# Kernel optimization log

Measured on AMD Instinct MI355X. Metric: run time of the kernel, lower is better.

## Reference

```python
import jax, jax.numpy as jnp
import numpy as np

B, NQ, NC, D, C = 8, 1024, 4096, 256, 24  # batch, n_query, n_context, emb_dim, num_classes


def setup_inputs() -> dict:
    key = jax.random.key(0)
    ks = jax.random.split(key, 11)
    sc = 0.05  # param init scale
    return {
        "q_head": jax.random.normal(ks[0], (B, NQ, D), jnp.float32),
        "q_tail": jax.random.normal(ks[1], (B, NQ, D), jnp.float32),
        "c_head": jax.random.normal(ks[2], (B, NC, D), jnp.float32),
        "c_tail": jax.random.normal(ks[3], (B, NC, D), jnp.float32),
        "context_labels": jax.random.randint(ks[4], (B, NC), 0, C + 1),
        "mask": jnp.ones((B, NC), jnp.float32),
        "W_rel": jax.random.normal(ks[5], (2 * D, D), jnp.float32) * sc,
        "b_rel": jnp.zeros((D,), jnp.float32),
        "W_gen": jax.random.normal(ks[6], (D, C + 1), jnp.float32) * sc,
        "b_gen": jnp.zeros((C + 1,), jnp.float32),
        "W_cp": jax.random.normal(ks[7], (2 * D, 1), jnp.float32) * sc,
        "b_cp": jnp.zeros((1,), jnp.float32),
    }


def reference(q_head, q_tail, c_head, c_tail, context_labels, mask,
              W_rel, b_rel, W_gen, b_gen, W_cp, b_cp):
    def rel_emb(h, t):
        return jnp.concatenate([h, t], axis=-1) @ W_rel + b_rel

    q_emb = rel_emb(q_head, q_tail)            # [B, NQ, D]
    c_emb = rel_emb(c_head, c_tail)            # [B, NC, D]

    # generate distribution
    gen_dist = jax.nn.log_softmax(q_emb @ W_gen + b_gen, axis=-1)  # [B, NQ, C+1]

    # attention distribution (copy)
    scores = jnp.einsum('bqd,bjd->bqj', q_emb, c_emb) * mask[:, None, :]  # [B, NQ, NC]
    lsm = jax.nn.log_softmax(scores, axis=-1)
    probs = jnp.exp(lsm)
    context_vec = jnp.einsum('bqj,bjd->bqd', probs, c_emb)  # [B, NQ, D]

    # grouped logsumexp over context labels == log(sum of softmax probs per class);
    # empty classes give log(0) = -inf, matching the original -inf mask + logsumexp.
    onehot = jax.nn.one_hot(context_labels, C + 1, dtype=probs.dtype)  # [B, NC, C+1]
    copy_dist = jnp.log(jnp.einsum('bqj,bjc->bqc', probs, onehot))     # [B, NQ, C+1]

    # should-copy gate
    logits = (jnp.concatenate([q_emb, context_vec], axis=-1) @ W_cp + b_cp)[..., 0]  # [B, NQ]
    copy_prob = jax.nn.log_sigmoid(logits)[..., None]
    gen_prob = jax.nn.log_sigmoid(-logits)[..., None]

    return jnp.logaddexp(copy_prob + copy_dist, gen_prob + gen_dist)  # [B, NQ, C+1]
```

## Files before the change

kernel.cpp:

```cpp
#include <hip/hip_runtime.h>


typedef __attribute__((ext_vector_type(8))) _Float16 half8;
typedef __attribute__((ext_vector_type(4))) float floatx4;

#define WB 8
#define WNQ 1024
#define WNC 4096
#define NROWS 8192

static __device__ __forceinline__ float logsig(float x) {
    return (x >= 0.f) ? -log1pf(__expf(-x)) : x - log1pf(__expf(x));
}

union V16h { int4 v; half8 h8; _Float16 h[8]; unsigned short s[8]; uint2 u2[2]; };
union F8   { float4 v[2]; float f[8]; };
union H4   { _Float16 h[4]; uint2 u; unsigned short s[4]; };

static __device__ __forceinline__ void async_lds16(const _Float16* g, _Float16* l) {
    __builtin_amdgcn_global_load_lds(
        (const __attribute__((address_space(1))) unsigned int*)g,
        (__attribute__((address_space(3))) unsigned int*)l,
        16, 0, 0);
}

__global__ void wprep_kernel(const float* __restrict__ Wrel,
                             const float* __restrict__ Wgen,
                             const float* __restrict__ Wcp,
                             _Float16* __restrict__ WT,
                             _Float16* __restrict__ GenB)
{
    const int bx = blockIdx.x;
    if (bx < 256) {
        const int n = bx;
        for (int k = threadIdx.x; k < 512; k += 256)
            WT[(long)n * 512 + k] = (_Float16)Wrel[(long)k * 256 + n];
    } else {
        const int n = bx - 256;
        const int k = threadIdx.x;
        float v = 0.f;
        if (n < 25)       v = Wgen[(long)k * 25 + n];
        else if (n == 25) v = Wcp[k];
        GenB[(long)n * 256 + k] = (_Float16)v;
    }
}

__global__ __launch_bounds__(256, 3) void emb_kernel(
    const float* __restrict__ q_head, const float* __restrict__ q_tail,
    const float* __restrict__ c_head, const float* __restrict__ c_tail,
    const _Float16* __restrict__ WT,
    const float* __restrict__ brel,
    _Float16* __restrict__ Qf, _Float16* __restrict__ Cf,
    _Float16* __restrict__ CfT)
{
    __shared__ _Float16 sA[2][2048];

    const int tid  = threadIdx.x;
    const int lane = tid & 63;
    const int wv   = tid >> 6;
    const int l15  = lane & 15;
    const int quad = lane >> 4;
    const int n0   = wv * 64;

    const float* head; const float* tail; _Float16* Ef;
    long m0; bool isQ;
    if (blockIdx.x < 128) {
        isQ = true;  head = q_head; tail = q_tail; Ef = Qf;
        m0 = (long)blockIdx.x * 64;
    } else {
        isQ = false; head = c_head; tail = c_tail; Ef = Cf;
        m0 = (long)(blockIdx.x - 128) * 64;
    }

    const long arow = m0 + (tid >> 2);
    const int  akc  = (tid & 3) * 8;

    floatx4 acc[4][4];
#pragma unroll
    for (int a = 0; a < 4; ++a)
#pragma unroll
        for (int bq = 0; bq < 4; ++bq) acc[a][bq] = (floatx4)(0.0f);

    F8 aCur;
    aCur.v[0] = *(const float4*)(head + arow * 256 + akc);
    aCur.v[1] = *(const float4*)(head + arow * 256 + akc + 4);
    V16h wCur[4];
#pragma unroll
    for (int nt = 0; nt < 4; ++nt)
        wCur[nt].v = *(const int4*)(WT + (long)(n0 + nt * 16 + l15) * 512 + quad * 8);

    for (int ks = 0; ks < 16; ++ks) {
        {
            V16h hp;
#pragma unroll
            for (int i = 0; i < 8; ++i) hp.h[i] = (_Float16)aCur.f[i];
            *(int4*)&sA[ks & 1][tid * 8] = hp.v;
        }
        F8 aNxt; V16h wNxt[4];
        if (ks < 15) {
            const int kg = (ks + 1) * 32;
            const float* srcb = (kg < 256) ? (head + kg) : (tail + (kg - 256));
            aNxt.v[0] = *(const float4*)(srcb + arow * 256 + akc);
            aNxt.v[1] = *(const float4*)(srcb + arow * 256 + akc + 4);
#pragma unroll
            for (int nt = 0; nt < 4; ++nt)
                wNxt[nt].v = *(const int4*)(WT + (long)(n0 + nt * 16 + l15) * 512 + kg + quad * 8);
        } else {
            aNxt = aCur;
#pragma unroll
            for (int nt = 0; nt < 4; ++nt) wNxt[nt] = wCur[nt];
        }
        __syncthreads();

        V16h af[4];
#pragma unroll
        for (int mb = 0; mb < 4; ++mb)
            af[mb].v = *(const int4*)&sA[ks & 1][(mb * 16 + l15) * 32 + quad * 8];
#pragma unroll
        for (int mb = 0; mb < 4; ++mb)
#pragma unroll
            for (int nt = 0; nt < 4; ++nt)
                acc[mb][nt] = __builtin_amdgcn_mfma_f32_16x16x32_f16(af[mb].h8, wCur[nt].h8, acc[mb][nt], 0, 0, 0);

        aCur = aNxt;
#pragma unroll
        for (int nt = 0; nt < 4; ++nt) wCur[nt] = wNxt[nt];
    }

    float bias[4];
#pragma unroll
    for (int nt = 0; nt < 4; ++nt) bias[nt] = brel[n0 + nt * 16 + l15];

    const int bidx = (int)(m0 >> 12);
    const int jc0  = (int)(m0 & 4095);
#pragma unroll
    for (int mb = 0; mb < 4; ++mb)
#pragma unroll
        for (int nt = 0; nt < 4; ++nt)
#pragma unroll
            for (int r = 0; r < 4; ++r) {
                const long row = m0 + mb * 16 + quad * 4 + r;
                const _Float16 h = (_Float16)(acc[mb][nt][r] + bias[nt]);
                Ef[row * 256 + n0 + nt * 16 + l15] = h;
                if (!isQ) {
                    const int jc = jc0 + mb * 16 + quad * 4 + r;
                    CfT[(long)bidx * 1048576 + (long)(n0 + nt * 16 + l15) * 4096 + jc] = h;
                }
            }
}

__global__ __launch_bounds__(256, 4) void gen_kernel(
    const _Float16* __restrict__ Qf,
    const _Float16* __restrict__ GenB,
    const float* __restrict__ bgen,
    float* __restrict__ genlog)
{
    const int tid  = threadIdx.x;
    const int lane = tid & 63;
    const int wv   = tid >> 6;
    const int l15  = lane & 15;
    const int quad = lane >> 4;
    const long m0  = (long)blockIdx.x * 64 + wv * 16;

    floatx4 acc[2];
    acc[0] = (floatx4)(0.0f); acc[1] = (floatx4)(0.0f);
#pragma unroll
    for (int ks = 0; ks < 8; ++ks) {
        V16h a, b0, b1;
        a.v  = *(const int4*)(Qf + (m0 + l15) * 256 + ks * 32 + quad * 8);
        b0.v = *(const int4*)(GenB + (long)(l15)      * 256 + ks * 32 + quad * 8);
        b1.v = *(const int4*)(GenB + (long)(16 + l15) * 256 + ks * 32 + quad * 8);
        acc[0] = __builtin_amdgcn_mfma_f32_16x16x32_f16(a.h8, b0.h8, acc[0], 0, 0, 0);
        acc[1] = __builtin_amdgcn_mfma_f32_16x16x32_f16(a.h8, b1.h8, acc[1], 0, 0, 0);
    }
#pragma unroll
    for (int nt = 0; nt < 2; ++nt) {
        const int col = nt * 16 + l15;
        const float bias = (col < 25) ? bgen[col] : 0.f;
#pragma unroll
        for (int r = 0; r < 4; ++r)
            genlog[(m0 + quad * 4 + r) * 32 + col] = acc[nt][r] + bias;
    }
}

__global__ __launch_bounds__(256, 2) void attn_kernel(
    const _Float16* __restrict__ qf,
    const _Float16* __restrict__ cf,
    const _Float16* __restrict__ cfT,
    const int*      __restrict__ labels,
    const float*    __restrict__ maskp,
    unsigned short* __restrict__ Oh,
    float* __restrict__ Mst,
    float* __restrict__ Lst,
    int jtiles, int nsh)
{
    __shared__ _Float16 sA[2][8192];
    __shared__ _Float16 sB[2][8192];
    __shared__ _Float16 Pw[4][16 * 40];

    const int tid  = threadIdx.x;
    const int lane = tid & 63;
    const int wv   = tid >> 6;
    const int l15  = lane & 15;
    const int quad = lane >> 4;

    const int f   = blockIdx.x;
    const int xcd = f & 7;
    const int seq = f >> 3;
    const int qt  = seq & 15;
    const int u   = seq >> 4;
    const int pr  = u * 8 + xcd;
    const int b   = pr >> nsh;
    const int sp  = pr & ((1 << nsh) - 1);
    const int q0  = qt * 64;

    V16h qfr[8];
    {
        const long qrow = (long)b * WNQ + q0 + wv * 16 + l15;
#pragma unroll
        for (int ks = 0; ks < 8; ++ks)
            qfr[ks].v = *(const int4*)(qf + qrow * 256 + ks * 32 + quad * 8);
    }

    floatx4 O[18];
#pragma unroll
    for (int i = 0; i < 18; ++i) O[i] = (floatx4)(0.0f);
    float m_run = -INFINITY, l_run = 0.f;

    const int jb0 = sp * (jtiles * 32);

    auto stage = [&](int bf, int jb) {
        const long cbase = ((long)b * WNC + jb) * 256;
#pragma unroll
        for (int t = 0; t < 4; ++t) {
            const int idx = wv * 4 + t;
            const int ks = idx >> 1, jh = idx & 1;
            async_lds16(cf + cbase + (jh * 16 + l15) * 256 + ks * 32 + quad * 8,
                        &sA[bf][idx * 512]);
        }
        const long tbase = (long)b * 1048576 + jb;
#pragma unroll
        for (int t = 0; t < 4; ++t) {
            const int W = wv * 4 + t;
            async_lds16(cfT + tbase + (long)(W * 16 + (lane >> 2)) * 4096 + (lane & 3) * 8,
                        &sB[bf][W * 512]);
        }
    };

    stage(0, jb0);

    for (int it = 0; it < jtiles; ++it) {
        const int cur = it & 1;
        const int jb  = jb0 + it * 32;
        __syncthreads();
        if (it + 1 < jtiles) stage(cur ^ 1, jb + 32);

        const float4 mv0 = *(const float4*)(maskp + (long)b * WNC + jb + quad * 4);
        const float4 mv1 = *(const float4*)(maskp + (long)b * WNC + jb + 16 + quad * 4);
        const int4 lb0 = *(const int4*)(labels + (long)b * WNC + jb + quad * 8);
        const int4 lb1 = *(const int4*)(labels + (long)b * WNC + jb + quad * 8 + 4);

        floatx4 accS0 = (floatx4)(0.0f), accS1 = (floatx4)(0.0f);
#pragma unroll
        for (int ks = 0; ks < 8; ++ks) {
            V16h a0, a1;
            a0.v = *(const int4*)&sA[cur][(ks * 2 + 0) * 512 + (quad * 16 + l15) * 8];
            a1.v = *(const int4*)&sA[cur][(ks * 2 + 1) * 512 + (quad * 16 + l15) * 8];
            accS0 = __builtin_amdgcn_mfma_f32_16x16x32_f16(a0.h8, qfr[ks].h8, accS0, 0, 0, 0);
            accS1 = __builtin_amdgcn_mfma_f32_16x16x32_f16(a1.h8, qfr[ks].h8, accS1, 0, 0, 0);
        }
        const float* mv0p = (const float*)&mv0;
        const float* mv1p = (const float*)&mv1;
#pragma unroll
        for (int r = 0; r < 4; ++r) {
            accS0[r] *= mv0p[r];
            accS1[r] *= mv1p[r];
        }

        float v = fmaxf(fmaxf(fmaxf(accS0[0], accS0[1]), fmaxf(accS0[2], accS0[3])),
                        fmaxf(fmaxf(accS1[0], accS1[1]), fmaxf(accS1[2], accS1[3])));
        v = fmaxf(v, __shfl_xor(v, 16, 64));
        v = fmaxf(v, __shfl_xor(v, 32, 64));
        const float m_new = fmaxf(m_run, v);
        const float alpha = __expf(m_run - m_new);
        float p[8]; float ts = 0.f;
#pragma unroll
        for (int r = 0; r < 4; ++r) {
            p[r]     = __expf(accS0[r] - m_new); ts += p[r];
            p[4 + r] = __expf(accS1[r] - m_new); ts += p[4 + r];
        }
        ts += __shfl_xor(ts, 16, 64);
        ts += __shfl_xor(ts, 32, 64);
        l_run = l_run * alpha + ts;
        m_run = m_new;

        float ar[4];
#pragma unroll
        for (int r = 0; r < 4; ++r) ar[r] = __shfl(alpha, quad * 4 + r, 64);
#pragma unroll
        for (int fo = 0; fo < 18; ++fo)
#pragma unroll
            for (int r = 0; r < 4; ++r) O[fo][r] *= ar[r];

#pragma unroll
        for (int jf = 0; jf < 2; ++jf) {
            H4 w;
#pragma unroll
            for (int r = 0; r < 4; ++r) w.h[r] = (_Float16)p[jf * 4 + r];
            *(uint2*)&Pw[wv][l15 * 40 + jf * 16 + quad * 4] = w.u;
        }
        asm volatile("" ::: "memory");
        V16h pf;
        pf.v = *(const int4*)&Pw[wv][l15 * 40 + quad * 8];

        const int* lbp0 = (const int*)&lb0;
        const int* lbp1 = (const int*)&lb1;
        V16h oh0, oh1;
#pragma unroll
        for (int i = 0; i < 8; ++i) {
            const int lv = (i < 4) ? lbp0[i] : lbp1[i - 4];
            oh0.h[i] = (lv == l15)        ? (_Float16)1.0f : (_Float16)0.0f;
            oh1.h[i] = (lv == (l15 + 16)) ? (_Float16)1.0f : (_Float16)0.0f;
        }

#pragma unroll
        for (int dt = 0; dt < 16; ++dt) {
            V16h bfr;
            bfr.v = *(const int4*)&sB[cur][((dt * 16 + l15) * 4 + quad) * 8];
            O[dt] = __builtin_amdgcn_mfma_f32_16x16x32_f16(pf.h8, bfr.h8, O[dt], 0, 0, 0);
        }
        O[16] = __builtin_amdgcn_mfma_f32_16x16x32_f16(pf.h8, oh0.h8, O[16], 0, 0, 0);
        O[17] = __builtin_amdgcn_mfma_f32_16x16x32_f16(pf.h8, oh1.h8, O[17], 0, 0, 0);
    }

    {
        const long orow0 = (long)(sp * WB + b) * WNQ + q0 + wv * 16;
#pragma unroll
        for (int dt = 0; dt < 18; ++dt)
#pragma unroll
            for (int r = 0; r < 4; ++r) {
                H4 h; h.h[0] = (_Float16)O[dt][r];
                Oh[(orow0 + quad * 4 + r) * 288 + dt * 16 + l15] = h.s[0];
            }
        if (lane < 16) {
            const long sidx = (long)(sp * WB + b) * WNQ + q0 + wv * 16 + lane;
            Mst[sidx] = m_run;
            Lst[sidx] = l_run;
        }
    }
}

__global__ __launch_bounds__(256) void final_kernel(
    const float* __restrict__ genlog,
    const unsigned short* __restrict__ Oh,
    const float* __restrict__ Mst,
    const float* __restrict__ Lst,
    const float* __restrict__ Wcp,
    const float* __restrict__ bcp,
    float* __restrict__ outp,
    int ns)
{
    __shared__ float gA[4][32];
    __shared__ float cdA[4][32];

    const int tid  = threadIdx.x;
    const int lane = tid & 63;
    const int wv   = tid >> 6;
    const int row  = blockIdx.x * 4 + wv;

    float ms[8];
#pragma unroll
    for (int s = 0; s < 8; ++s) ms[s] = (s < ns) ? Mst[(long)s * NROWS + row] : -INFINITY;
    float mstar = -INFINITY;
#pragma unroll
    for (int s = 0; s < 8; ++s) mstar = fmaxf(mstar, ms[s]);
    float wgt[8]; float L = 0.f;
#pragma unroll
    for (int s = 0; s < 8; ++s) {
        wgt[s] = (ms[s] == -INFINITY) ? 0.f : __expf(ms[s] - mstar);
        if (s < ns) L += Lst[(long)s * NROWS + row] * wgt[s];
    }

    const int d0 = lane * 4;
    float ctx[4] = {0.f, 0.f, 0.f, 0.f};
#pragma unroll
    for (int s = 0; s < 8; ++s) {
        if (s < ns) {
            H4 t; t.u = *(const uint2*)&Oh[((long)s * NROWS + row) * 288 + d0];
#pragma unroll
            for (int i = 0; i < 4; ++i) ctx[i] += wgt[s] * (float)t.h[i];
        }
    }

    float cls[4] = {0.f, 0.f, 0.f, 0.f};
    if (lane < 8) {
#pragma unroll
        for (int s = 0; s < 8; ++s) {
            if (s < ns) {
                H4 t; t.u = *(const uint2*)&Oh[((long)s * NROWS + row) * 288 + 256 + lane * 4];
#pragma unroll
                for (int i = 0; i < 4; ++i) cls[i] += wgt[s] * (float)t.h[i];
            }
        }
    }

    float g = (lane < 25) ? genlog[(long)row * 32 + lane] : -INFINITY;
    float mg = g;
#pragma unroll
    for (int off = 32; off >= 1; off >>= 1) mg = fmaxf(mg, __shfl_xor(mg, off, 64));
    float se = (lane < 25) ? __expf(g - mg) : 0.f;
#pragma unroll
    for (int off = 32; off >= 1; off >>= 1) se += __shfl_xor(se, off, 64);
    const float glsm = g - mg - logf(se);

    const float qgate = genlog[(long)row * 32 + 25];
    const float invL = 1.f / L;
    float part = 0.f;
#pragma unroll
    for (int i = 0; i < 4; ++i)
        part += ctx[i] * invL * Wcp[256 + d0 + i];
#pragma unroll
    for (int off = 32; off >= 1; off >>= 1) part += __shfl_xor(part, off, 64);
    const float logit = qgate + part + bcp[0];

    const float lscp  = logsig(logit);
    const float lsgen = logsig(-logit);
    const float logL  = logf(L);

    if (lane < 8) {
#pragma unroll
        for (int i = 0; i < 4; ++i)
            cdA[wv][lane * 4 + i] = (cls[i] > 0.f) ? (logf(cls[i]) - logL) : -INFINITY;
    }
    if (lane < 25) gA[wv][lane] = glsm;
    __syncthreads();

    if (lane < 25) {
        const float a  = lscp + cdA[wv][lane];
        const float bb = lsgen + gA[wv][lane];
        const float mx = fmaxf(a, bb);
        const float o  = (mx == -INFINITY) ? -INFINITY
                         : mx + log1pf(__expf(fminf(a, bb) - mx));
        outp[(long)row * 25 + lane] = o;
    }
}

extern "C" void kernel_launch(void* const* d_in, const int* in_sizes, int n_in,
                              void* d_out, int out_size, void* d_ws, size_t ws_size,
                              hipStream_t stream) {
    const float* q_head = (const float*)d_in[0];
    const float* q_tail = (const float*)d_in[1];
    const float* c_head = (const float*)d_in[2];
    const float* c_tail = (const float*)d_in[3];
    const int*   labels = (const int*)d_in[4];
    const float* maskp  = (const float*)d_in[5];
    const float* Wrel   = (const float*)d_in[6];
    const float* brel   = (const float*)d_in[7];
    const float* Wgen   = (const float*)d_in[8];
    const float* bgen   = (const float*)d_in[9];
    const float* Wcp    = (const float*)d_in[10];
    const float* bcp    = (const float*)d_in[11];

    auto need = [](long ns) -> long { return 39075840l + ns * 4784128l; };
    int ns = 8, nsh = 3;
    if ((long)ws_size < need(8)) { ns = 4; nsh = 2; }
    if ((long)ws_size < need(4)) { ns = 2; nsh = 1; }
    if ((long)ws_size < need(2)) { ns = 1; nsh = 0; }
    const int jtiles = 128 / ns;

    char* ws = (char*)d_ws;
    _Float16* Qf     = (_Float16*)(ws);
    _Float16* Cf     = (_Float16*)(ws + 4194304l);
    _Float16* CfT    = (_Float16*)(ws + 20971520l);
    _Float16* WT     = (_Float16*)(ws + 37748736l);
    _Float16* GenB   = (_Float16*)(ws + 38010880l);
    float*    genlog = (float*)   (ws + 38027264l);
    unsigned short* Oh = (unsigned short*)(ws + 39075840l);
    float*    Mst    = (float*)   (ws + 39075840l + (long)ns * 4718592l);
    float*    Lst    = Mst + (long)ns * NROWS;

    hipLaunchKernelGGL(wprep_kernel, dim3(288), dim3(256), 0, stream,
                       Wrel, Wgen, Wcp, WT, GenB);
    hipLaunchKernelGGL(emb_kernel, dim3(640), dim3(256), 0, stream,
                       q_head, q_tail, c_head, c_tail, WT, brel, Qf, Cf, CfT);
    hipLaunchKernelGGL(gen_kernel, dim3(128), dim3(256), 0, stream,
                       Qf, GenB, bgen, genlog);
    hipLaunchKernelGGL(attn_kernel, dim3(16 * 8 * ns), dim3(256), 0, stream,
                       Qf, Cf, CfT, labels, maskp, Oh, Mst, Lst, jtiles, nsh);
    hipLaunchKernelGGL(final_kernel, dim3(NROWS / 4), dim3(256), 0, stream,
                       genlog, Oh, Mst, Lst, Wcp, bcp, (float*)d_out, ns);
}
```

Before: 288.2 us.

## Stage CfT transpose through LDS, widen attention blocks, skip redundant rescales

The embedding kernel now buffers the context-embedding tile in a swizzled LDS array and writes the transposed copy as coalesced 16-byte stores, replacing scattered 2-byte transposed stores. The attention kernel goes from 256 to 512 threads, with each block covering 128 query rows, so every staged context tile in LDS feeds twice as many waves and each wave issues half as many async loads. The output-accumulator rescale is skipped when no lane's running max changed. In exchange the embedding kernel uses more LDS and a barrier, and the larger attention blocks at launch bound 4 may hit register or occupancy limits.

```diff
diff --git a/kernel.cpp b/kernel.cpp
--- a/kernel.cpp
+++ b/kernel.cpp
@@ -54,6 +54,7 @@
     _Float16* __restrict__ CfT)
 {
     __shared__ _Float16 sA[2][2048];
+    __shared__ _Float16 sO[256 * 64];
 
     const int tid  = threadIdx.x;
     const int lane = tid & 63;
@@ -131,22 +132,42 @@
 #pragma unroll
     for (int nt = 0; nt < 4; ++nt) bias[nt] = brel[n0 + nt * 16 + l15];
 
-    const int bidx = (int)(m0 >> 12);
-    const int jc0  = (int)(m0 & 4095);
 #pragma unroll
     for (int mb = 0; mb < 4; ++mb)
 #pragma unroll
-        for (int nt = 0; nt < 4; ++nt)
+        for (int nt = 0; nt < 4; ++nt) {
+            H4 hq;
 #pragma unroll
             for (int r = 0; r < 4; ++r) {
                 const long row = m0 + mb * 16 + quad * 4 + r;
                 const _Float16 h = (_Float16)(acc[mb][nt][r] + bias[nt]);
                 Ef[row * 256 + n0 + nt * 16 + l15] = h;
-                if (!isQ) {
-                    const int jc = jc0 + mb * 16 + quad * 4 + r;
-                    CfT[(long)bidx * 1048576 + (long)(n0 + nt * 16 + l15) * 4096 + jc] = h;
-                }
+                hq.h[r] = h;
             }
+            if (!isQ) {
+                const int n  = n0 + nt * 16 + l15;
+                const int sw = (mb * 4 + quad) ^ l15;
+                *(uint2*)&sO[n * 64 + sw * 4] = hq.u;
+            }
+        }
+
+    if (!isQ) {
+        __syncthreads();
+        const int bidx = (int)(m0 >> 12);
+        const int jc0  = (int)(m0 & 4095);
+        const int c    = tid & 7;
+        const int nl   = tid >> 3;
+#pragma unroll
+        for (int i = 0; i < 8; ++i) {
+            const int n  = nl + 32 * i;
+            const int s0 = (2 * c)     ^ (n & 15);
+            const int s1 = (2 * c + 1) ^ (n & 15);
+            const uint2 u0 = *(const uint2*)&sO[n * 64 + s0 * 4];
+            const uint2 u1 = *(const uint2*)&sO[n * 64 + s1 * 4];
+            int4 out; out.x = u0.x; out.y = u0.y; out.z = u1.x; out.w = u1.y;
+            *(int4*)&CfT[(long)bidx * 1048576 + (long)n * 4096 + jc0 + c * 8] = out;
+        }
+    }
 }
 
 __global__ __launch_bounds__(256, 4) void gen_kernel(
@@ -183,7 +204,7 @@
     }
 }
 
-__global__ __launch_bounds__(256, 2) void attn_kernel(
+__global__ __launch_bounds__(512, 4) void attn_kernel(
     const _Float16* __restrict__ qf,
     const _Float16* __restrict__ cf,
     const _Float16* __restrict__ cfT,
@@ -196,7 +217,7 @@
 {
     __shared__ _Float16 sA[2][8192];
     __shared__ _Float16 sB[2][8192];
-    __shared__ _Float16 Pw[4][16 * 40];
+    __shared__ _Float16 Pw[8][16 * 40];
 
     const int tid  = threadIdx.x;
     const int lane = tid & 63;
@@ -207,12 +228,12 @@
     const int f   = blockIdx.x;
     const int xcd = f & 7;
     const int seq = f >> 3;
-    const int qt  = seq & 15;
-    const int u   = seq >> 4;
+    const int qt  = seq & 7;
+    const int u   = seq >> 3;
     const int pr  = u * 8 + xcd;
     const int b   = pr >> nsh;
     const int sp  = pr & ((1 << nsh) - 1);
-    const int q0  = qt * 64;
+    const int q0  = qt * 128;
 
     V16h qfr[8];
     {
@@ -232,16 +253,16 @@
     auto stage = [&](int bf, int jb) {
         const long cbase = ((long)b * WNC + jb) * 256;
 #pragma unroll
-        for (int t = 0; t < 4; ++t) {
-            const int idx = wv * 4 + t;
+        for (int t = 0; t < 2; ++t) {
+            const int idx = wv * 2 + t;
             const int ks = idx >> 1, jh = idx & 1;
             async_lds16(cf + cbase + (jh * 16 + l15) * 256 + ks * 32 + quad * 8,
                         &sA[bf][idx * 512]);
         }
         const long tbase = (long)b * 1048576 + jb;
 #pragma unroll
-        for (int t = 0; t < 4; ++t) {
-            const int W = wv * 4 + t;
+        for (int t = 0; t < 2; ++t) {
+            const int W = wv * 2 + t;
             async_lds16(cfT + tbase + (long)(W * 16 + (lane >> 2)) * 4096 + (lane & 3) * 8,
                         &sB[bf][W * 512]);
         }
@@ -282,6 +303,7 @@
         v = fmaxf(v, __shfl_xor(v, 16, 64));
         v = fmaxf(v, __shfl_xor(v, 32, 64));
         const float m_new = fmaxf(m_run, v);
+        const bool upd = __any(m_new > m_run);
         const float alpha = __expf(m_run - m_new);
         float p[8]; float ts = 0.f;
 #pragma unroll
@@ -294,13 +316,15 @@
         l_run = l_run * alpha + ts;
         m_run = m_new;
 
-        float ar[4];
-#pragma unroll
-        for (int r = 0; r < 4; ++r) ar[r] = __shfl(alpha, quad * 4 + r, 64);
-#pragma unroll
-        for (int fo = 0; fo < 18; ++fo)
-#pragma unroll
-            for (int r = 0; r < 4; ++r) O[fo][r] *= ar[r];
+        if (upd) {
+            float ar[4];
+#pragma unroll
+            for (int r = 0; r < 4; ++r) ar[r] = __shfl(alpha, quad * 4 + r, 64);
+#pragma unroll
+            for (int fo = 0; fo < 18; ++fo)
+#pragma unroll
+                for (int r = 0; r < 4; ++r) O[fo][r] *= ar[r];
+        }
 
 #pragma unroll
         for (int jf = 0; jf < 2; ++jf) {
@@ -485,7 +509,7 @@
                        q_head, q_tail, c_head, c_tail, WT, brel, Qf, Cf, CfT);
     hipLaunchKernelGGL(gen_kernel, dim3(128), dim3(256), 0, stream,
                        Qf, GenB, bgen, genlog);
-    hipLaunchKernelGGL(attn_kernel, dim3(16 * 8 * ns), dim3(256), 0, stream,
+    hipLaunchKernelGGL(attn_kernel, dim3(64 * ns), dim3(512), 0, stream,
                        Qf, Cf, CfT, labels, maskp, Oh, Mst, Lst, jtiles, nsh);
     hipLaunchKernelGGL(final_kernel, dim3(NROWS / 4), dim3(256), 0, stream,
                        genlog, Oh, Mst, Lst, Wcp, bcp, (float*)d_out, ns);
```

Result: slower. 435.8 us (+51.2%).
